# Optimization experiments

Hardware: AMD Instinct MI355X
Metric: run time of the kernel (lower is better)

## Reference

```python
import jax, jax.numpy as jnp
import numpy as np

TEMPERATURE = 1.0
B, D = 8192, 256


def setup_inputs() -> dict:
    key = jax.random.key(0)
    k1, k2 = jax.random.split(key)
    return {
        "encoder_embedding1": jax.random.normal(k1, (B, D), dtype=jnp.float32),
        "encoder_embedding2": jax.random.normal(k2, (B, D), dtype=jnp.float32),
    }


def _l2_normalize(x, eps=1e-8):
    # matches torch CosineSimilarity eps handling closely enough for fp32
    n = jnp.sqrt(jnp.sum(x * x, axis=-1, keepdims=True))
    return x / jnp.maximum(n, eps)


def reference(encoder_embedding1, encoder_embedding2):
    # sim[i, j] = cos(contrast_i, anchor_j); torch builds this via a (B,B,D)
    # expand + elementwise CosineSimilarity — here it's a normalized matmul.
    a = _l2_normalize(encoder_embedding1)  # anchors  [B, D]
    c = _l2_normalize(encoder_embedding2)  # contrast [B, D]
    sim = jnp.einsum("id,jd->ij", c, a)    # [B, B]
    log_probs = jax.nn.log_softmax(sim / TEMPERATURE, axis=0)
    loss = -jnp.sum(jnp.diagonal(log_probs)) * TEMPERATURE
    return loss
```

## Files before the change

kernel.cpp:

```cpp
#include <hip/hip_runtime.h>
#include <hip/hip_bf16.h>
#include <hip/hip_fp8.h>


#define BROWS 8192
#define DIM   256

typedef int   i32x4 __attribute__((ext_vector_type(4)));
typedef int   i32x8 __attribute__((ext_vector_type(8)));
typedef float f32x4 __attribute__((ext_vector_type(4)));

__device__ __forceinline__ void gload_lds16(const void* g, void* l) {
  __builtin_amdgcn_global_load_lds(
      (const __attribute__((address_space(1))) unsigned int*)g,
      (__attribute__((address_space(3))) unsigned int*)l, 16, 0, 0);
}

__device__ __forceinline__ unsigned char to_e4m3(float v) {
  __hip_fp8_e4m3 t(v);
  return *reinterpret_cast<unsigned char*>(&t);
}

__global__ __launch_bounds__(256) void prep_kernel(
    const float* __restrict__ E1, const float* __restrict__ E2,
    unsigned char* __restrict__ An8, unsigned char* __restrict__ Cn8,
    float* __restrict__ diag, float* __restrict__ colsum) {
  if (blockIdx.x < 32) colsum[blockIdx.x * 256 + threadIdx.x] = 0.f;

  const int w    = threadIdx.x >> 6;
  const int lane = threadIdx.x & 63;
  const int row  = blockIdx.x * 4 + w;
  const size_t base = (size_t)row * DIM + lane * 4;

  const float4 a = *(const float4*)(E1 + base);
  const float4 c = *(const float4*)(E2 + base);

  float sa  = a.x*a.x + a.y*a.y + a.z*a.z + a.w*a.w;
  float sc  = c.x*c.x + c.y*c.y + c.z*c.z + c.w*c.w;
  float sac = a.x*c.x + a.y*c.y + a.z*c.z + a.w*c.w;
#pragma unroll
  for (int o = 32; o > 0; o >>= 1) {
    sa  += __shfl_down(sa,  o);
    sc  += __shfl_down(sc,  o);
    sac += __shfl_down(sac, o);
  }
  const float inva = 1.0f / fmaxf(sqrtf(__shfl(sa, 0)), 1e-8f);
  const float invc = 1.0f / fmaxf(sqrtf(__shfl(sc, 0)), 1e-8f);

  uchar4 pa, pc;
  pa.x = to_e4m3(a.x * inva); pa.y = to_e4m3(a.y * inva);
  pa.z = to_e4m3(a.z * inva); pa.w = to_e4m3(a.w * inva);
  pc.x = to_e4m3(c.x * invc); pc.y = to_e4m3(c.y * invc);
  pc.z = to_e4m3(c.z * invc); pc.w = to_e4m3(c.w * invc);
  *(uchar4*)(An8 + base) = pa;
  *(uchar4*)(Cn8 + base) = pc;
  if (lane == 0) diag[row] = sac * inva * invc;
}

__global__ __launch_bounds__(256, 2) void gemm_colsum_kernel(
    const unsigned char* __restrict__ Cn8,
    const unsigned char* __restrict__ An8,
    float* __restrict__ colsum) {
  __shared__ __align__(16) unsigned char ldsC[128 * 256];
  __shared__ __align__(16) unsigned char ldsA[128 * 256];
  __shared__ float ldscol[2][128];

  const int tid  = threadIdx.x;
  const int lane = tid & 63;
  const int w    = tid >> 6;
  const int wr   = w >> 1;
  const int wc   = w & 1;

  const int jtile = blockIdx.x & 63;
  const int itile = blockIdx.x >> 6;
  const int i0 = itile * 128;
  const int j0 = jtile * 128;

  const int sr = tid >> 4;
  const int pl = (tid & 15) ^ (sr & 7);
  const unsigned char* gC = Cn8 + (size_t)(i0 + sr) * DIM + pl * 16;
  const unsigned char* gA = An8 + (size_t)(j0 + sr) * DIM + pl * 16;

#pragma unroll
  for (int j = 0; j < 8; ++j) {
    gload_lds16(gC + (size_t)j * 16 * DIM, &ldsC[0] + j * 4096 + w * 1024);
    gload_lds16(gA + (size_t)j * 16 * DIM, &ldsA[0] + j * 4096 + w * 1024);
  }
  asm volatile("s_waitcnt vmcnt(0)" ::: "memory");
  __builtin_amdgcn_sched_barrier(0);
  __builtin_amdgcn_s_barrier();

  f32x4 acc[4][4] = {};
  const int q  = lane >> 4;
  const int rb = lane & 15;
  const int SC = 0x7F7F7F7F;

#pragma unroll
  for (int W = 0; W < 2; ++W) {
    i32x8 af[4], bfv[4];
#pragma unroll
    for (int m = 0; m < 4; ++m) {
      const int r  = wr * 64 + m * 16 + rb;
      const int s0 = (W * 8 + q * 2)     ^ (r & 7);
      const int s1 = (W * 8 + q * 2 + 1) ^ (r & 7);
      union { i32x4 h[2]; i32x8 v; } u;
      u.h[0] = *(const i32x4*)(&ldsC[0] + r * 256 + s0 * 16);
      u.h[1] = *(const i32x4*)(&ldsC[0] + r * 256 + s1 * 16);
      af[m] = u.v;
    }
#pragma unroll
    for (int n = 0; n < 4; ++n) {
      const int r  = wc * 64 + n * 16 + rb;
      const int s0 = (W * 8 + q * 2)     ^ (r & 7);
      const int s1 = (W * 8 + q * 2 + 1) ^ (r & 7);
      union { i32x4 h[2]; i32x8 v; } u;
      u.h[0] = *(const i32x4*)(&ldsA[0] + r * 256 + s0 * 16);
      u.h[1] = *(const i32x4*)(&ldsA[0] + r * 256 + s1 * 16);
      bfv[n] = u.v;
    }
    __builtin_amdgcn_s_setprio(1);
#pragma unroll
    for (int m = 0; m < 4; ++m)
#pragma unroll
      for (int n = 0; n < 4; ++n)
        acc[m][n] = __builtin_amdgcn_mfma_scale_f32_16x16x128_f8f6f4(
            af[m], bfv[n], acc[m][n], 0 , 0 ,
            0, SC, 0, SC);
    __builtin_amdgcn_s_setprio(0);
  }

#pragma unroll
  for (int n = 0; n < 4; ++n) {
    float s = 0.f;
#pragma unroll
    for (int m = 0; m < 4; ++m) {
      const f32x4 v = acc[m][n];
      s += __expf(v[0]) + __expf(v[1]) + __expf(v[2]) + __expf(v[3]);
    }
    s += __shfl_xor(s, 16);
    s += __shfl_xor(s, 32);
    if (lane < 16) ldscol[wr][wc * 64 + n * 16 + lane] = s;
  }
  __syncthreads();
  if (tid < 128) {
    const float v = ldscol[0][tid] + ldscol[1][tid];
    atomicAdd(&colsum[j0 + tid], v);
  }
}

__global__ __launch_bounds__(256) void finalize_kernel(
    const float* __restrict__ colsum, const float* __restrict__ diag,
    float* __restrict__ out) {
  const int t = threadIdx.x;
  float s = 0.f;
  for (int j = t; j < BROWS; j += 256) s += logf(colsum[j]) - diag[j];
#pragma unroll
  for (int o = 32; o > 0; o >>= 1) s += __shfl_down(s, o);
  __shared__ float red[4];
  if ((t & 63) == 0) red[t >> 6] = s;
  __syncthreads();
  if (t == 0) out[0] = red[0] + red[1] + red[2] + red[3];
}

extern "C" void kernel_launch(void* const* d_in, const int* in_sizes, int n_in,
                              void* d_out, int out_size, void* d_ws, size_t ws_size,
                              hipStream_t stream) {
  const float* E1 = (const float*)d_in[0];
  const float* E2 = (const float*)d_in[1];
  char* ws = (char*)d_ws;
  unsigned char* Cn8 = (unsigned char*)(ws);
  unsigned char* An8 = (unsigned char*)(ws + (size_t)2 * 1024 * 1024);
  float* colsum = (float*)(ws + (size_t)4 * 1024 * 1024);
  float* diag   = (float*)(ws + (size_t)4 * 1024 * 1024 + 32 * 1024);
  float* out = (float*)d_out;

  prep_kernel<<<BROWS / 4, 256, 0, stream>>>(E1, E2, An8, Cn8, diag, colsum);
  gemm_colsum_kernel<<<(BROWS / 128) * (BROWS / 128), 256, 0, stream>>>(Cn8, An8, colsum);
  finalize_kernel<<<1, 256, 0, stream>>>(colsum, diag, out);
}
```

Before: 50.88 us.

## Make GEMM blocks persistent over 512 columns with double-buffered A tiles

Each GEMM block now keeps its 128-row C tile resident in LDS and loops over eight 64-column chunks of A. The A chunks are double-buffered with async global-to-LDS loads, so the next chunk's load overlaps the current chunk's MFMA and exp work. The grid shrinks from 4096 to 1024 blocks, which amortises C loads and launch overhead. In exchange, each block does more atomics (per wave, per chunk, with no LDS pre-reduction across the wr pair) and adds barriers each iteration, and parallelism per block falls with fewer blocks.

```diff
diff --git a/kernel.cpp b/kernel.cpp
--- a/kernel.cpp
+++ b/kernel.cpp
@@ -61,9 +61,8 @@
     const unsigned char* __restrict__ Cn8,
     const unsigned char* __restrict__ An8,
     float* __restrict__ colsum) {
-  __shared__ __align__(16) unsigned char ldsC[128 * 256];
-  __shared__ __align__(16) unsigned char ldsA[128 * 256];
-  __shared__ float ldscol[2][128];
+  __shared__ __align__(16) unsigned char ldsC[32768];
+  __shared__ __align__(16) unsigned char ldsA[2][16384];
 
   const int tid  = threadIdx.x;
   const int lane = tid & 63;
@@ -71,80 +70,113 @@
   const int wr   = w >> 1;
   const int wc   = w & 1;
 
-  const int jtile = blockIdx.x & 63;
-  const int itile = blockIdx.x >> 6;
+  const int jgroup = blockIdx.x & 15;
+  const int itile  = blockIdx.x >> 4;
   const int i0 = itile * 128;
-  const int j0 = jtile * 128;
+  const int j0 = jgroup * 512;
 
   const int sr = tid >> 4;
   const int pl = (tid & 15) ^ (sr & 7);
   const unsigned char* gC = Cn8 + (size_t)(i0 + sr) * DIM + pl * 16;
   const unsigned char* gA = An8 + (size_t)(j0 + sr) * DIM + pl * 16;
 
-#pragma unroll
-  for (int j = 0; j < 8; ++j) {
-    gload_lds16(gC + (size_t)j * 16 * DIM, &ldsC[0] + j * 4096 + w * 1024);
-    gload_lds16(gA + (size_t)j * 16 * DIM, &ldsA[0] + j * 4096 + w * 1024);
-  }
-  asm volatile("s_waitcnt vmcnt(0)" ::: "memory");
+  auto stageA = [&](int jj, int buf) {
+#pragma unroll
+    for (int r = 0; r < 4; ++r)
+      gload_lds16(gA + (size_t)(jj * 64 + r * 16) * DIM,
+                  &ldsA[buf][0] + r * 4096 + w * 1024);
+  };
+
+#pragma unroll
+  for (int r = 0; r < 8; ++r)
+    gload_lds16(gC + (size_t)(r * 16) * DIM, &ldsC[0] + r * 4096 + w * 1024);
+  stageA(0, 0);
+  stageA(1, 1);
+
+  asm volatile("s_waitcnt vmcnt(8)" ::: "memory");
   __builtin_amdgcn_sched_barrier(0);
   __builtin_amdgcn_s_barrier();
 
-  f32x4 acc[4][4] = {};
   const int q  = lane >> 4;
   const int rb = lane & 15;
   const int SC = 0x7F7F7F7F;
 
-#pragma unroll
-  for (int W = 0; W < 2; ++W) {
-    i32x8 af[4], bfv[4];
-#pragma unroll
-    for (int m = 0; m < 4; ++m) {
-      const int r  = wr * 64 + m * 16 + rb;
+  i32x8 af[4][2];
+#pragma unroll
+  for (int m = 0; m < 4; ++m) {
+    const int r = wr * 64 + m * 16 + rb;
+#pragma unroll
+    for (int W = 0; W < 2; ++W) {
       const int s0 = (W * 8 + q * 2)     ^ (r & 7);
       const int s1 = (W * 8 + q * 2 + 1) ^ (r & 7);
       union { i32x4 h[2]; i32x8 v; } u;
       u.h[0] = *(const i32x4*)(&ldsC[0] + r * 256 + s0 * 16);
       u.h[1] = *(const i32x4*)(&ldsC[0] + r * 256 + s1 * 16);
-      af[m] = u.v;
+      af[m][W] = u.v;
     }
-#pragma unroll
-    for (int n = 0; n < 4; ++n) {
-      const int r  = wc * 64 + n * 16 + rb;
-      const int s0 = (W * 8 + q * 2)     ^ (r & 7);
-      const int s1 = (W * 8 + q * 2 + 1) ^ (r & 7);
-      union { i32x4 h[2]; i32x8 v; } u;
-      u.h[0] = *(const i32x4*)(&ldsA[0] + r * 256 + s0 * 16);
-      u.h[1] = *(const i32x4*)(&ldsA[0] + r * 256 + s1 * 16);
-      bfv[n] = u.v;
+  }
+  asm volatile("s_waitcnt lgkmcnt(0)" ::: "memory");
+  __builtin_amdgcn_sched_barrier(0);
+
+#pragma unroll
+  for (int jj = 0; jj < 8; ++jj) {
+    const int b = jj & 1;
+    if (jj == 0)      asm volatile("s_waitcnt vmcnt(4)" ::: "memory");
+    else if (jj == 1) asm volatile("s_waitcnt vmcnt(6)" ::: "memory");
+    else if (jj == 7) asm volatile("s_waitcnt vmcnt(4)" ::: "memory");
+    else              asm volatile("s_waitcnt vmcnt(8)" ::: "memory");
+    __builtin_amdgcn_sched_barrier(0);
+    __builtin_amdgcn_s_barrier();
+
+    i32x8 bf[2][2];
+#pragma unroll
+    for (int n = 0; n < 2; ++n) {
+      const int r = wc * 32 + n * 16 + rb;
+#pragma unroll
+      for (int W = 0; W < 2; ++W) {
+        const int s0 = (W * 8 + q * 2)     ^ (r & 7);
+        const int s1 = (W * 8 + q * 2 + 1) ^ (r & 7);
+        union { i32x4 h[2]; i32x8 v; } u;
+        u.h[0] = *(const i32x4*)(&ldsA[b][0] + r * 256 + s0 * 16);
+        u.h[1] = *(const i32x4*)(&ldsA[b][0] + r * 256 + s1 * 16);
+        bf[n][W] = u.v;
+      }
     }
+    asm volatile("s_waitcnt lgkmcnt(0)" ::: "memory");
+    __builtin_amdgcn_sched_barrier(0);
+    __builtin_amdgcn_s_barrier();
+    __builtin_amdgcn_sched_barrier(0);
+
+    if (jj < 6) stageA(jj + 2, b);
+    __builtin_amdgcn_sched_barrier(0);
+
+    f32x4 acc[4][2] = {};
     __builtin_amdgcn_s_setprio(1);
 #pragma unroll
     for (int m = 0; m < 4; ++m)
 #pragma unroll
-      for (int n = 0; n < 4; ++n)
-        acc[m][n] = __builtin_amdgcn_mfma_scale_f32_16x16x128_f8f6f4(
-            af[m], bfv[n], acc[m][n], 0 , 0 ,
-            0, SC, 0, SC);
+      for (int n = 0; n < 2; ++n)
+#pragma unroll
+        for (int W = 0; W < 2; ++W)
+          acc[m][n] = __builtin_amdgcn_mfma_scale_f32_16x16x128_f8f6f4(
+              af[m][W], bf[n][W], acc[m][n], 0, 0, 0, SC, 0, SC);
     __builtin_amdgcn_s_setprio(0);
-  }
-
-#pragma unroll
-  for (int n = 0; n < 4; ++n) {
-    float s = 0.f;
-#pragma unroll
-    for (int m = 0; m < 4; ++m) {
-      const f32x4 v = acc[m][n];
-      s += __expf(v[0]) + __expf(v[1]) + __expf(v[2]) + __expf(v[3]);
+    __builtin_amdgcn_sched_barrier(0);
+
+#pragma unroll
+    for (int n = 0; n < 2; ++n) {
+      float s = 0.f;
+#pragma unroll
+      for (int m = 0; m < 4; ++m) {
+        const f32x4 v = acc[m][n];
+        s += __expf(v[0]) + __expf(v[1]) + __expf(v[2]) + __expf(v[3]);
+      }
+      s += __shfl_xor(s, 16);
+      s += __shfl_xor(s, 32);
+      if (lane < 16)
+        atomicAdd(&colsum[j0 + jj * 64 + wc * 32 + n * 16 + lane], s);
     }
-    s += __shfl_xor(s, 16);
-    s += __shfl_xor(s, 32);
-    if (lane < 16) ldscol[wr][wc * 64 + n * 16 + lane] = s;
-  }
-  __syncthreads();
-  if (tid < 128) {
-    const float v = ldscol[0][tid] + ldscol[1][tid];
-    atomicAdd(&colsum[j0 + tid], v);
+    __builtin_amdgcn_sched_barrier(0);
   }
 }
 
@@ -175,6 +207,6 @@
   float* out = (float*)d_out;
 
   prep_kernel<<<BROWS / 4, 256, 0, stream>>>(E1, E2, An8, Cn8, diag, colsum);
-  gemm_colsum_kernel<<<(BROWS / 128) * (BROWS / 128), 256, 0, stream>>>(Cn8, An8, colsum);
+  gemm_colsum_kernel<<<64 * 16, 256, 0, stream>>>(Cn8, An8, colsum);
   finalize_kernel<<<1, 256, 0, stream>>>(colsum, diag, out);
 }
```

After: 46.27 us (median of 2 runs). 9.1% less time.
